# Performance work log

Hardware: AMD Instinct MI355X
Metric: run time of the kernel (lower is better)

Reference implementation:

```python
import jax, jax.numpy as jnp
import numpy as np
import math

KERNEL_SIZES = [3, 5, 7, 7, 9, 9]
DILATIONS = [1, 2, 1, 3, 1, 2]
NUM_HEADS = 6
HEAD_DIM = 32  # in_channels 192 / 6 heads


def _neighborhood_patches(t, k, dil):
    """Equivalent of F.unfold(t, kernel_size=k, dilation=dil, padding=dil*(k//2)).
    t: [B, d, H, W] -> [B, d, k*k, H, W] (zero-padded borders, torch unfold ordering:
    patch index p = i*k + j over the kernel window, row-major)."""
    B, d, H, W = t.shape
    pad = dil * (k // 2)
    tp = jnp.pad(t, ((0, 0), (0, 0), (pad, pad), (pad, pad)))
    pats = [tp[:, :, i * dil:i * dil + H, j * dil:j * dil + W]
            for i in range(k) for j in range(k)]
    return jnp.stack(pats, axis=2)


def setup_inputs() -> dict:
    key = jax.random.key(0)
    ks = jax.random.split(key, 3 + NUM_HEADS)
    B, C, H, W = 4, 192, 96, 96
    x = jax.random.normal(ks[0], (B, C, H, W), dtype=jnp.float32)
    w_qkv = jax.random.normal(ks[1], (3 * C, C), dtype=jnp.float32) * 0.02  # 1x1 conv weight
    w_out = jax.random.normal(ks[2], (C, C), dtype=jnp.float32) * 0.02      # 1x1 conv weight
    inp = {"x": x, "w_qkv": w_qkv, "w_out": w_out}
    for i, k in enumerate(KERNEL_SIZES):
        # module inits biases to zeros; use small randn so softmax path is exercised
        inp[f"b{i}"] = jax.random.normal(ks[3 + i], (k * k,), dtype=jnp.float32) * 0.02
    return inp


def reference(x, w_qkv, w_out, b0, b1, b2, b3, b4, b5):
    biases = [b0, b1, b2, b3, b4, b5]
    B, C, H, W = x.shape
    scale = 1.0 / math.sqrt(HEAD_DIM)
    # 1x1 conv qkv projection
    qkv = jnp.einsum('bchw,oc->bohw', x, w_qkv)
    q, k, v = jnp.split(qkv, 3, axis=1)
    q = q.reshape(B, NUM_HEADS, HEAD_DIM, H, W)
    k = k.reshape(B, NUM_HEADS, HEAD_DIM, H, W)
    v = v.reshape(B, NUM_HEADS, HEAD_DIM, H, W)
    head_outs = []
    for i in range(NUM_HEADS):  # heads have structurally different (k, dilation)
        ksz, dil = KERNEL_SIZES[i], DILATIONS[i]
        kp = _neighborhood_patches(k[:, i], ksz, dil)  # [B, d, k*k, H, W]
        vp = _neighborhood_patches(v[:, i], ksz, dil)  # [B, d, k*k, H, W]
        scores = jnp.einsum('bdhw,bdphw->bphw', q[:, i], kp) * scale
        scores = scores + biases[i][None, :, None, None]
        attn = jax.nn.softmax(scores, axis=1)  # softmax over the k*k neighborhood
        head_outs.append(jnp.einsum('bphw,bdphw->bdhw', attn, vp))
    out = jnp.concatenate(head_outs, axis=1)  # [B, C, H, W]
    return jnp.einsum('bchw,oc->bohw', out, w_out)
```

## Files before the change

### kernel.cpp

```cpp
#include <hip/hip_runtime.h>
#include <hip/hip_bf16.h>
#include <math.h>

#define NPIX 9216
#define HDIM 96
#define WDIM 96
#define NHEADS 6
#define BATCH 4

typedef __bf16 bf16x8 __attribute__((ext_vector_type(8)));
typedef float  f32x4  __attribute__((ext_vector_type(4)));

struct Bias6 { const float* p[6]; };

__device__ __forceinline__ void cp16(void* ldst, const void* gsrc) {
    __builtin_amdgcn_global_load_lds(
        (const __attribute__((address_space(1))) unsigned int*)gsrc,
        (__attribute__((address_space(3))) unsigned int*)ldst, 16, 0, 0);
}

__device__ __forceinline__ unsigned short bfbits(__bf16 x) { return *(unsigned short*)&x; }

__device__ __forceinline__ unsigned packf16(float a, float b) {
    _Float16 ha = (_Float16)a, hb = (_Float16)b;
    return (unsigned)*(unsigned short*)&ha | ((unsigned)*(unsigned short*)&hb << 16);
}

#define MIX_LL(acc, kk, qq) asm("v_fma_mix_f32 %0, %1, %2, %0 op_sel:[0,0,0] op_sel_hi:[1,1,0]" : "+v"(acc) : "v"(kk), "v"(qq))
#define MIX_HH(acc, kk, qq) asm("v_fma_mix_f32 %0, %1, %2, %0 op_sel:[1,1,0] op_sel_hi:[1,1,0]" : "+v"(acc) : "v"(kk), "v"(qq))
#define MIX_LF(acc, vv, ee) asm("v_fma_mix_f32 %0, %1, %2, %0 op_sel:[0,0,0] op_sel_hi:[1,0,0]" : "+v"(acc) : "v"(vv), "v"(ee))
#define MIX_HF(acc, vv, ee) asm("v_fma_mix_f32 %0, %1, %2, %0 op_sel:[1,0,0] op_sel_hi:[1,0,0]" : "+v"(acc) : "v"(vv), "v"(ee))

__global__ __launch_bounds__(256) void convert_w(
    const float* __restrict__ w1, __bf16* __restrict__ h1, __bf16* __restrict__ l1, int n1,
    const float* __restrict__ w2, __bf16* __restrict__ h2, __bf16* __restrict__ l2, int n2)
{
    const int i = blockIdx.x * 256 + threadIdx.x;
    if (i < n1) { float f = w1[i]; __bf16 h = (__bf16)f; h1[i] = h; l1[i] = (__bf16)(f - (float)h); }
    if (i < n2) { float f = w2[i]; __bf16 h = (__bf16)f; h2[i] = h; l2[i] = (__bf16)(f - (float)h); }
}

__global__ __launch_bounds__(256) void convert_x(
    const float* __restrict__ x, __bf16* __restrict__ Xh)
{
    __shared__ float t[32][65];
    const int b  = blockIdx.z;
    const int c0 = blockIdx.y * 32;
    const int p0 = blockIdx.x * 64;
    const int tid = threadIdx.x;
    const int pl = tid & 63;
    #pragma unroll
    for (int i = 0; i < 8; ++i) {
        const int c = i * 4 + (tid >> 6);
        t[c][pl] = x[((size_t)b * 192 + c0 + c) * NPIX + p0 + pl];
    }
    __syncthreads();
    const int p  = tid >> 2;
    const int cq = (tid & 3) * 8;
    bf16x8 vh;
    #pragma unroll
    for (int j = 0; j < 8; ++j)
        vh[j] = (__bf16)t[cq + j][p];
    *(bf16x8*)(Xh + ((size_t)b * NPIX + p0 + p) * 192 + c0 + cq) = vh;
}

template<int MODE>
__global__ __launch_bounds__(256) void gemm_mfma(
    const __bf16* __restrict__ Ah, const __bf16* __restrict__ Al,
    const __bf16* __restrict__ Bh,
    void* __restrict__ Yv, int M)
{
    __shared__ __bf16 sAh[64 * 64];
    __shared__ __bf16 sAl[64 * 64];
    __shared__ __bf16 sBh[128 * 64];

    const int b  = blockIdx.z;
    const int n0 = blockIdx.x * 128;
    const int m0 = blockIdx.y * 64;
    const int tid  = threadIdx.x;
    const int lane = tid & 63;
    const int wid  = tid >> 6;
    const int wr = wid >> 1, wc = wid & 1;
    const int lr = lane & 15;
    const int kg = lane >> 4;

    const char* gA_h = (const char*)Ah + (size_t)m0 * 384;
    const char* gA_l = (const char*)Al + (size_t)m0 * 384;
    const char* gB   = (const char*)Bh + ((size_t)b * NPIX + n0) * 384;

    f32x4 acc[2][4];
    #pragma unroll
    for (int mf = 0; mf < 2; ++mf)
        #pragma unroll
        for (int nf = 0; nf < 4; ++nf)
            acc[mf][nf] = (f32x4){0.f, 0.f, 0.f, 0.f};

    for (int ks = 0; ks < 3; ++ks) {
        if (ks) __syncthreads();
        const int kb = ks * 128;
        #pragma unroll
        for (int it = 0; it < 2; ++it) {
            const int d  = it * 256 + tid;
            const int rd = d >> 3, cd = d & 7;
            const size_t src = (size_t)rd * 384 + kb + ((cd ^ (rd & 7)) << 4);
            cp16((char*)sAh + d * 16, gA_h + src);
            cp16((char*)sAl + d * 16, gA_l + src);
        }
        #pragma unroll
        for (int it = 0; it < 4; ++it) {
            const int d  = it * 256 + tid;
            const int rd = d >> 3, cd = d & 7;
            const size_t src = (size_t)rd * 384 + kb + ((cd ^ (rd & 7)) << 4);
            cp16((char*)sBh + d * 16, gB + src);
        }
        __syncthreads();
        #pragma unroll
        for (int s = 0; s < 2; ++s) {
            bf16x8 aH[2], aL[2], bH[4];
            #pragma unroll
            for (int mf = 0; mf < 2; ++mf) {
                const int row = wr * 32 + mf * 16 + lr;
                const int c = (s * 4 + kg) ^ (row & 7);
                aH[mf] = *(const bf16x8*)((const char*)sAh + row * 128 + c * 16);
                aL[mf] = *(const bf16x8*)((const char*)sAl + row * 128 + c * 16);
            }
            #pragma unroll
            for (int nf = 0; nf < 4; ++nf) {
                const int row = wc * 64 + nf * 16 + lr;
                const int c = (s * 4 + kg) ^ (row & 7);
                bH[nf] = *(const bf16x8*)((const char*)sBh + row * 128 + c * 16);
            }
            #pragma unroll
            for (int mf = 0; mf < 2; ++mf)
                #pragma unroll
                for (int nf = 0; nf < 4; ++nf) {
                    acc[mf][nf] = __builtin_amdgcn_mfma_f32_16x16x32_bf16(aH[mf], bH[nf], acc[mf][nf], 0, 0, 0);
                    acc[mf][nf] = __builtin_amdgcn_mfma_f32_16x16x32_bf16(aL[mf], bH[nf], acc[mf][nf], 0, 0, 0);
                }
        }
    }

    if (MODE == 0) {
        float* Yb = (float*)Yv + ((size_t)b * M + m0 + wr * 32) * NPIX + n0 + wc * 64;
        #pragma unroll
        for (int mf = 0; mf < 2; ++mf)
            #pragma unroll
            for (int r = 0; r < 4; ++r) {
                const int row = mf * 16 + kg * 4 + r;
                #pragma unroll
                for (int nf = 0; nf < 4; ++nf)
                    Yb[(size_t)row * NPIX + nf * 16 + lr] = acc[mf][nf][r];
            }
    } else {
        #pragma unroll
        for (int mf = 0; mf < 2; ++mf) {
            const int mbase = m0 + wr * 32 + mf * 16 + kg * 4;
            unsigned* Yb = (unsigned*)Yv + ((size_t)b * (M >> 1) + (mbase >> 1)) * NPIX
                         + n0 + wc * 64 + lr;
            #pragma unroll
            for (int nf = 0; nf < 4; ++nf) {
                Yb[nf * 16]        = packf16(acc[mf][nf][0], acc[mf][nf][1]);
                Yb[(size_t)NPIX + nf * 16] = packf16(acc[mf][nf][2], acc[mf][nf][3]);
            }
        }
    }
}

#define MAX_REGION 1300

template<int KSZ, int DIL>
__device__ __forceinline__ void attn_body(
    const unsigned* __restrict__ Qpp, const unsigned* __restrict__ Kpp,
    const unsigned* __restrict__ Vpp, const float* __restrict__ bias,
    __bf16* __restrict__ oh, int h0, int w0,
    uint4* __restrict__ lds,
    unsigned (* __restrict__ out_lds)[256])
{
    constexpr int CC  = KSZ / 2;
    constexpr int HAL = CC * DIL;
    constexpr int R   = 8 + 2 * HAL;
    constexpr int C   = 32 + 2 * HAL;
    constexpr int RC  = R * C;
    constexpr int NN  = KSZ * KSZ;
    const float scale = 0.17677669529663689f;

    const int tx = threadIdx.x & 31;
    const int ty = threadIdx.x >> 5;
    const int pix = (h0 + ty) * WDIM + (w0 + tx);
    const int lb = ty * C + tx;

    float score[NN];
    #pragma unroll
    for (int n = 0; n < NN; ++n) score[n] = 0.f;

    for (int pp = 0; pp < 16; pp += 4) {
        __syncthreads();
        for (int idx = threadIdx.x; idx < RC; idx += 256) {
            const int r = idx / C, c = idx - r * C;
            const int gh = h0 - HAL + r, gw = w0 - HAL + c;
            uint4 v = make_uint4(0u, 0u, 0u, 0u);
            if ((unsigned)gh < (unsigned)HDIM && (unsigned)gw < (unsigned)WDIM) {
                const unsigned* p = Kpp + (size_t)pp * NPIX + gh * WDIM + gw;
                v.x = p[0 * NPIX];
                v.y = p[1 * NPIX];
                v.z = p[2 * NPIX];
                v.w = p[3 * NPIX];
            }
            lds[idx] = v;
        }
        __syncthreads();
        unsigned qp0 = Qpp[(size_t)(pp + 0) * NPIX + pix];
        unsigned qp1 = Qpp[(size_t)(pp + 1) * NPIX + pix];
        unsigned qp2 = Qpp[(size_t)(pp + 2) * NPIX + pix];
        unsigned qp3 = Qpp[(size_t)(pp + 3) * NPIX + pix];
        #pragma unroll
        for (int i = 0; i < KSZ; ++i)
            #pragma unroll
            for (int j = 0; j < KSZ; ++j) {
                const uint4 k8 = lds[lb + i * DIL * C + j * DIL];
                float s = score[i * KSZ + j];
                MIX_LL(s, k8.x, qp0); MIX_HH(s, k8.x, qp0);
                MIX_LL(s, k8.y, qp1); MIX_HH(s, k8.y, qp1);
                MIX_LL(s, k8.z, qp2); MIX_HH(s, k8.z, qp2);
                MIX_LL(s, k8.w, qp3); MIX_HH(s, k8.w, qp3);
                score[i * KSZ + j] = s;
            }
    }

    float l = 0.f;
    #pragma unroll
    for (int n = 0; n < NN; ++n) {
        const float e = __expf(score[n] * scale + bias[n]);
        l += e;
        score[n] = e;
    }
    const float inv = 1.f / l;

    for (int pp = 0; pp < 16; pp += 4) {
        __syncthreads();
        for (int idx = threadIdx.x; idx < RC; idx += 256) {
            const int r = idx / C, c = idx - r * C;
            const int gh = h0 - HAL + r, gw = w0 - HAL + c;
            uint4 v = make_uint4(0u, 0u, 0u, 0u);
            if ((unsigned)gh < (unsigned)HDIM && (unsigned)gw < (unsigned)WDIM) {
                const unsigned* p = Vpp + (size_t)pp * NPIX + gh * WDIM + gw;
                v.x = p[0 * NPIX];
                v.y = p[1 * NPIX];
                v.z = p[2 * NPIX];
                v.w = p[3 * NPIX];
            }
            lds[idx] = v;
        }
        __syncthreads();
        float a0 = 0.f, a1 = 0.f, a2 = 0.f, a3 = 0.f;
        float a4 = 0.f, a5 = 0.f, a6 = 0.f, a7 = 0.f;
        #pragma unroll
        for (int i = 0; i < KSZ; ++i)
            #pragma unroll
            for (int j = 0; j < KSZ; ++j) {
                const uint4 v8 = lds[lb + i * DIL * C + j * DIL];
                const float e = score[i * KSZ + j];
                MIX_LF(a0, v8.x, e); MIX_HF(a1, v8.x, e);
                MIX_LF(a2, v8.y, e); MIX_HF(a3, v8.y, e);
                MIX_LF(a4, v8.z, e); MIX_HF(a5, v8.z, e);
                MIX_LF(a6, v8.w, e); MIX_HF(a7, v8.w, e);
            }
        const __bf16 c0 = (__bf16)(a0 * inv), c1 = (__bf16)(a1 * inv);
        const __bf16 c2 = (__bf16)(a2 * inv), c3 = (__bf16)(a3 * inv);
        const __bf16 c4 = (__bf16)(a4 * inv), c5 = (__bf16)(a5 * inv);
        const __bf16 c6 = (__bf16)(a6 * inv), c7 = (__bf16)(a7 * inv);
        out_lds[pp + 0][threadIdx.x] = (unsigned)bfbits(c0) | ((unsigned)bfbits(c1) << 16);
        out_lds[pp + 1][threadIdx.x] = (unsigned)bfbits(c2) | ((unsigned)bfbits(c3) << 16);
        out_lds[pp + 2][threadIdx.x] = (unsigned)bfbits(c4) | ((unsigned)bfbits(c5) << 16);
        out_lds[pp + 3][threadIdx.x] = (unsigned)bfbits(c6) | ((unsigned)bfbits(c7) << 16);
    }

    __syncthreads();
    #pragma unroll
    for (int it = 0; it < 4; ++it) {
        const int linear = it * 256 + threadIdx.x;
        const int px = linear >> 2;
        const int c  = linear & 3;
        const int gpix = (h0 + (px >> 5)) * WDIM + w0 + (px & 31);
        uint4 val = make_uint4(out_lds[c * 4 + 0][px], out_lds[c * 4 + 1][px],
                               out_lds[c * 4 + 2][px], out_lds[c * 4 + 3][px]);
        *(uint4*)((unsigned*)(oh + (size_t)gpix * 192) + c * 4) = val;
    }
}

__global__ __launch_bounds__(256) void attn_kernel(
    const unsigned* __restrict__ qkv, Bias6 bs, __bf16* __restrict__ ATh)
{
    __shared__ uint4 lds[MAX_REGION];
    __shared__ unsigned out_lds[16][256];

    const int orig = blockIdx.x;
    const int wg = (orig & 7) * 108 + (orig >> 3);
    const int panel = wg / 36;
    const int tile = wg - panel * 36;
    const int chunk = panel / 3, slot = panel - chunk * 3;
    int head, b;
    if (slot == 0)      { head = 4 + (chunk >> 2); b = chunk & 3; }
    else if (slot == 1) { head = 2 + (chunk >> 2); b = chunk & 3; }
    else                { head = (chunk < 4) ? 1 : 0; b = chunk & 3; }
    const int tx = tile % 3, ty = tile / 3;
    const int w0 = tx * 32, h0 = ty * 8;

    const unsigned* Qpp = qkv + ((size_t)b * 288 + head * 16) * NPIX;
    const unsigned* Kpp = Qpp + (size_t)96 * NPIX;
    const unsigned* Vpp = Qpp + (size_t)192 * NPIX;
    __bf16* oh = ATh + (size_t)b * NPIX * 192 + head * 32;
    const float* bias = bs.p[head];

    switch (head) {
        case 0: attn_body<3, 1>(Qpp, Kpp, Vpp, bias, oh, h0, w0, lds, out_lds); break;
        case 1: attn_body<5, 2>(Qpp, Kpp, Vpp, bias, oh, h0, w0, lds, out_lds); break;
        case 2: attn_body<7, 1>(Qpp, Kpp, Vpp, bias, oh, h0, w0, lds, out_lds); break;
        case 3: attn_body<7, 3>(Qpp, Kpp, Vpp, bias, oh, h0, w0, lds, out_lds); break;
        case 4: attn_body<9, 1>(Qpp, Kpp, Vpp, bias, oh, h0, w0, lds, out_lds); break;
        case 5: attn_body<9, 2>(Qpp, Kpp, Vpp, bias, oh, h0, w0, lds, out_lds); break;
    }
}

extern "C" void kernel_launch(void* const* d_in, const int* in_sizes, int n_in,
                              void* d_out, int out_size, void* d_ws, size_t ws_size,
                              hipStream_t stream) {
    const float* x     = (const float*)d_in[0];
    const float* w_qkv = (const float*)d_in[1];
    const float* w_out = (const float*)d_in[2];
    Bias6 bs;
    for (int i = 0; i < 6; ++i) bs.p[i] = (const float*)d_in[3 + i];
    float* out = (float*)d_out;

    char* ws = (char*)d_ws;
    unsigned* QKV = (unsigned*)ws;      ws += (size_t)BATCH * 288 * NPIX * 4;
    __bf16* Xh  = (__bf16*)ws;          ws += (size_t)BATCH * NPIX * 192 * 2;
    __bf16* ATh = (__bf16*)ws;          ws += (size_t)BATCH * NPIX * 192 * 2;
    __bf16* W1h = (__bf16*)ws;          ws += (size_t)576 * 192 * 2;
    __bf16* W1l = (__bf16*)ws;          ws += (size_t)576 * 192 * 2;
    __bf16* W2h = (__bf16*)ws;          ws += (size_t)192 * 192 * 2;
    __bf16* W2l = (__bf16*)ws;          ws += (size_t)192 * 192 * 2;

    convert_w<<<dim3((576 * 192 + 255) / 256), 256, 0, stream>>>(
        w_qkv, W1h, W1l, 576 * 192, w_out, W2h, W2l, 192 * 192);
    convert_x<<<dim3(NPIX / 64, 192 / 32, BATCH), 256, 0, stream>>>(x, Xh);

    gemm_mfma<1><<<dim3(NPIX / 128, 576 / 64, BATCH), 256, 0, stream>>>(
        W1h, W1l, Xh, (void*)QKV, 576);

    attn_kernel<<<dim3(864), 256, 0, stream>>>(QKV, bs, ATh);

    gemm_mfma<0><<<dim3(NPIX / 128, 192 / 64, BATCH), 256, 0, stream>>>(
        W2h, W2l, ATh, (void*)out, 192);
}
```

Measured before the change: 98.98 us.

## Store QKV as 8-channel interleaved uint4 planes for vectorized attention loads

The QKV GEMM epilogue now writes fp16 pairs into a layout where each pixel holds 8 consecutive channels in one 16-byte chunk. The attention kernel then fetches K, V and Q neighborhoods with single uint4 loads instead of four strided 4-byte loads. It also halves the output staging buffer by writing results in two halves, which costs extra barriers. The GEMM stores become strided 4-byte writes with a 16-byte stride, which may be less coalesced.

Measured after the change: 97.38 us. Within noise of the previous version (-1.6%).

```diff
diff --git a/kernel.cpp b/kernel.cpp
--- a/kernel.cpp
+++ b/kernel.cpp
@@ -154,13 +154,14 @@
     } else {
         #pragma unroll
         for (int mf = 0; mf < 2; ++mf) {
-            const int mbase = m0 + wr * 32 + mf * 16 + kg * 4;
-            unsigned* Yb = (unsigned*)Yv + ((size_t)b * (M >> 1) + (mbase >> 1)) * NPIX
-                         + n0 + wc * 64 + lr;
+            const int cbase = m0 + wr * 32 + mf * 16 + kg * 4;
+            unsigned* Yq = (unsigned*)Yv
+                + (((size_t)b * 72 + (cbase >> 3)) * NPIX + n0 + wc * 64 + lr) * 4
+                + ((kg & 1) << 1);
             #pragma unroll
             for (int nf = 0; nf < 4; ++nf) {
-                Yb[nf * 16]        = packf16(acc[mf][nf][0], acc[mf][nf][1]);
-                Yb[(size_t)NPIX + nf * 16] = packf16(acc[mf][nf][2], acc[mf][nf][3]);
+                Yq[(nf * 16) * 4 + 0] = packf16(acc[mf][nf][0], acc[mf][nf][1]);
+                Yq[(nf * 16) * 4 + 1] = packf16(acc[mf][nf][2], acc[mf][nf][3]);
             }
         }
     }
@@ -170,8 +171,8 @@
 
 template<int KSZ, int DIL>
 __device__ __forceinline__ void attn_body(
-    const unsigned* __restrict__ Qpp, const unsigned* __restrict__ Kpp,
-    const unsigned* __restrict__ Vpp, const float* __restrict__ bias,
+    const uint4* __restrict__ Qq, const uint4* __restrict__ Kq,
+    const uint4* __restrict__ Vq, const float* __restrict__ bias,
     __bf16* __restrict__ oh, int h0, int w0,
     uint4* __restrict__ lds,
     unsigned (* __restrict__ out_lds)[256])
@@ -193,36 +194,28 @@
     #pragma unroll
     for (int n = 0; n < NN; ++n) score[n] = 0.f;
 
-    for (int pp = 0; pp < 16; pp += 4) {
+    for (int pp = 0; pp < 4; ++pp) {
         __syncthreads();
         for (int idx = threadIdx.x; idx < RC; idx += 256) {
             const int r = idx / C, c = idx - r * C;
             const int gh = h0 - HAL + r, gw = w0 - HAL + c;
             uint4 v = make_uint4(0u, 0u, 0u, 0u);
-            if ((unsigned)gh < (unsigned)HDIM && (unsigned)gw < (unsigned)WDIM) {
-                const unsigned* p = Kpp + (size_t)pp * NPIX + gh * WDIM + gw;
-                v.x = p[0 * NPIX];
-                v.y = p[1 * NPIX];
-                v.z = p[2 * NPIX];
-                v.w = p[3 * NPIX];
-            }
+            if ((unsigned)gh < (unsigned)HDIM && (unsigned)gw < (unsigned)WDIM)
+                v = Kq[(size_t)pp * NPIX + gh * WDIM + gw];
             lds[idx] = v;
         }
         __syncthreads();
-        unsigned qp0 = Qpp[(size_t)(pp + 0) * NPIX + pix];
-        unsigned qp1 = Qpp[(size_t)(pp + 1) * NPIX + pix];
-        unsigned qp2 = Qpp[(size_t)(pp + 2) * NPIX + pix];
-        unsigned qp3 = Qpp[(size_t)(pp + 3) * NPIX + pix];
+        const uint4 qv = Qq[(size_t)pp * NPIX + pix];
         #pragma unroll
         for (int i = 0; i < KSZ; ++i)
             #pragma unroll
             for (int j = 0; j < KSZ; ++j) {
                 const uint4 k8 = lds[lb + i * DIL * C + j * DIL];
                 float s = score[i * KSZ + j];
-                MIX_LL(s, k8.x, qp0); MIX_HH(s, k8.x, qp0);
-                MIX_LL(s, k8.y, qp1); MIX_HH(s, k8.y, qp1);
-                MIX_LL(s, k8.z, qp2); MIX_HH(s, k8.z, qp2);
-                MIX_LL(s, k8.w, qp3); MIX_HH(s, k8.w, qp3);
+                MIX_LL(s, k8.x, qv.x); MIX_HH(s, k8.x, qv.x);
+                MIX_LL(s, k8.y, qv.y); MIX_HH(s, k8.y, qv.y);
+                MIX_LL(s, k8.z, qv.z); MIX_HH(s, k8.z, qv.z);
+                MIX_LL(s, k8.w, qv.w); MIX_HH(s, k8.w, qv.w);
                 score[i * KSZ + j] = s;
             }
     }
@@ -236,63 +229,62 @@
     }
     const float inv = 1.f / l;
 
-    for (int pp = 0; pp < 16; pp += 4) {
+    #pragma unroll
+    for (int half = 0; half < 2; ++half) {
+        #pragma unroll
+        for (int rr = 0; rr < 2; ++rr) {
+            const int pp = half * 2 + rr;
+            __syncthreads();
+            for (int idx = threadIdx.x; idx < RC; idx += 256) {
+                const int r = idx / C, c = idx - r * C;
+                const int gh = h0 - HAL + r, gw = w0 - HAL + c;
+                uint4 v = make_uint4(0u, 0u, 0u, 0u);
+                if ((unsigned)gh < (unsigned)HDIM && (unsigned)gw < (unsigned)WDIM)
+                    v = Vq[(size_t)pp * NPIX + gh * WDIM + gw];
+                lds[idx] = v;
+            }
+            __syncthreads();
+            float a0 = 0.f, a1 = 0.f, a2 = 0.f, a3 = 0.f;
+            float a4 = 0.f, a5 = 0.f, a6 = 0.f, a7 = 0.f;
+            #pragma unroll
+            for (int i = 0; i < KSZ; ++i)
+                #pragma unroll
+                for (int j = 0; j < KSZ; ++j) {
+                    const uint4 v8 = lds[lb + i * DIL * C + j * DIL];
+                    const float e = score[i * KSZ + j];
+                    MIX_LF(a0, v8.x, e); MIX_HF(a1, v8.x, e);
+                    MIX_LF(a2, v8.y, e); MIX_HF(a3, v8.y, e);
+                    MIX_LF(a4, v8.z, e); MIX_HF(a5, v8.z, e);
+                    MIX_LF(a6, v8.w, e); MIX_HF(a7, v8.w, e);
+                }
+            const __bf16 c0 = (__bf16)(a0 * inv), c1 = (__bf16)(a1 * inv);
+            const __bf16 c2 = (__bf16)(a2 * inv), c3 = (__bf16)(a3 * inv);
+            const __bf16 c4 = (__bf16)(a4 * inv), c5 = (__bf16)(a5 * inv);
+            const __bf16 c6 = (__bf16)(a6 * inv), c7 = (__bf16)(a7 * inv);
+            out_lds[rr * 4 + 0][threadIdx.x] = (unsigned)bfbits(c0) | ((unsigned)bfbits(c1) << 16);
+            out_lds[rr * 4 + 1][threadIdx.x] = (unsigned)bfbits(c2) | ((unsigned)bfbits(c3) << 16);
+            out_lds[rr * 4 + 2][threadIdx.x] = (unsigned)bfbits(c4) | ((unsigned)bfbits(c5) << 16);
+            out_lds[rr * 4 + 3][threadIdx.x] = (unsigned)bfbits(c6) | ((unsigned)bfbits(c7) << 16);
+        }
         __syncthreads();
-        for (int idx = threadIdx.x; idx < RC; idx += 256) {
-            const int r = idx / C, c = idx - r * C;
-            const int gh = h0 - HAL + r, gw = w0 - HAL + c;
-            uint4 v = make_uint4(0u, 0u, 0u, 0u);
-            if ((unsigned)gh < (unsigned)HDIM && (unsigned)gw < (unsigned)WDIM) {
-                const unsigned* p = Vpp + (size_t)pp * NPIX + gh * WDIM + gw;
-                v.x = p[0 * NPIX];
-                v.y = p[1 * NPIX];
-                v.z = p[2 * NPIX];
-                v.w = p[3 * NPIX];
-            }
-            lds[idx] = v;
-        }
-        __syncthreads();
-        float a0 = 0.f, a1 = 0.f, a2 = 0.f, a3 = 0.f;
-        float a4 = 0.f, a5 = 0.f, a6 = 0.f, a7 = 0.f;
-        #pragma unroll
-        for (int i = 0; i < KSZ; ++i)
-            #pragma unroll
-            for (int j = 0; j < KSZ; ++j) {
-                const uint4 v8 = lds[lb + i * DIL * C + j * DIL];
-                const float e = score[i * KSZ + j];
-                MIX_LF(a0, v8.x, e); MIX_HF(a1, v8.x, e);
-                MIX_LF(a2, v8.y, e); MIX_HF(a3, v8.y, e);
-                MIX_LF(a4, v8.z, e); MIX_HF(a5, v8.z, e);
-                MIX_LF(a6, v8.w, e); MIX_HF(a7, v8.w, e);
-            }
-        const __bf16 c0 = (__bf16)(a0 * inv), c1 = (__bf16)(a1 * inv);
-        const __bf16 c2 = (__bf16)(a2 * inv), c3 = (__bf16)(a3 * inv);
-        const __bf16 c4 = (__bf16)(a4 * inv), c5 = (__bf16)(a5 * inv);
-        const __bf16 c6 = (__bf16)(a6 * inv), c7 = (__bf16)(a7 * inv);
-        out_lds[pp + 0][threadIdx.x] = (unsigned)bfbits(c0) | ((unsigned)bfbits(c1) << 16);
-        out_lds[pp + 1][threadIdx.x] = (unsigned)bfbits(c2) | ((unsigned)bfbits(c3) << 16);
-        out_lds[pp + 2][threadIdx.x] = (unsigned)bfbits(c4) | ((unsigned)bfbits(c5) << 16);
-        out_lds[pp + 3][threadIdx.x] = (unsigned)bfbits(c6) | ((unsigned)bfbits(c7) << 16);
-    }
-
-    __syncthreads();
-    #pragma unroll
-    for (int it = 0; it < 4; ++it) {
-        const int linear = it * 256 + threadIdx.x;
-        const int px = linear >> 2;
-        const int c  = linear & 3;
-        const int gpix = (h0 + (px >> 5)) * WDIM + w0 + (px & 31);
-        uint4 val = make_uint4(out_lds[c * 4 + 0][px], out_lds[c * 4 + 1][px],
-                               out_lds[c * 4 + 2][px], out_lds[c * 4 + 3][px]);
-        *(uint4*)((unsigned*)(oh + (size_t)gpix * 192) + c * 4) = val;
+        #pragma unroll
+        for (int it = 0; it < 2; ++it) {
+            const int linear = it * 256 + threadIdx.x;
+            const int px = linear >> 1;
+            const int c  = linear & 1;
+            const int gpix = (h0 + (px >> 5)) * WDIM + w0 + (px & 31);
+            uint4 val = make_uint4(out_lds[c * 4 + 0][px], out_lds[c * 4 + 1][px],
+                                   out_lds[c * 4 + 2][px], out_lds[c * 4 + 3][px]);
+            *((uint4*)((unsigned*)(oh + (size_t)gpix * 192)) + half * 2 + c) = val;
+        }
     }
 }
 
 __global__ __launch_bounds__(256) void attn_kernel(
-    const unsigned* __restrict__ qkv, Bias6 bs, __bf16* __restrict__ ATh)
+    const uint4* __restrict__ qkv, Bias6 bs, __bf16* __restrict__ ATh)
 {
     __shared__ uint4 lds[MAX_REGION];
-    __shared__ unsigned out_lds[16][256];
+    __shared__ unsigned out_lds[8][256];
 
     const int orig = blockIdx.x;
     const int wg = (orig & 7) * 108 + (orig >> 3);
@@ -306,19 +298,20 @@
     const int tx = tile % 3, ty = tile / 3;
     const int w0 = tx * 32, h0 = ty * 8;
 
-    const unsigned* Qpp = qkv + ((size_t)b * 288 + head * 16) * NPIX;
-    const unsigned* Kpp = Qpp + (size_t)96 * NPIX;
-    const unsigned* Vpp = Qpp + (size_t)192 * NPIX;
+    const uint4* base = qkv + (size_t)b * 72 * NPIX;
+    const uint4* Qq = base + (size_t)(head * 4) * NPIX;
+    const uint4* Kq = base + (size_t)(24 + head * 4) * NPIX;
+    const uint4* Vq = base + (size_t)(48 + head * 4) * NPIX;
     __bf16* oh = ATh + (size_t)b * NPIX * 192 + head * 32;
     const float* bias = bs.p[head];
 
     switch (head) {
-        case 0: attn_body<3, 1>(Qpp, Kpp, Vpp, bias, oh, h0, w0, lds, out_lds); break;
-        case 1: attn_body<5, 2>(Qpp, Kpp, Vpp, bias, oh, h0, w0, lds, out_lds); break;
-        case 2: attn_body<7, 1>(Qpp, Kpp, Vpp, bias, oh, h0, w0, lds, out_lds); break;
-        case 3: attn_body<7, 3>(Qpp, Kpp, Vpp, bias, oh, h0, w0, lds, out_lds); break;
-        case 4: attn_body<9, 1>(Qpp, Kpp, Vpp, bias, oh, h0, w0, lds, out_lds); break;
-        case 5: attn_body<9, 2>(Qpp, Kpp, Vpp, bias, oh, h0, w0, lds, out_lds); break;
+        case 0: attn_body<3, 1>(Qq, Kq, Vq, bias, oh, h0, w0, lds, out_lds); break;
+        case 1: attn_body<5, 2>(Qq, Kq, Vq, bias, oh, h0, w0, lds, out_lds); break;
+        case 2: attn_body<7, 1>(Qq, Kq, Vq, bias, oh, h0, w0, lds, out_lds); break;
+        case 3: attn_body<7, 3>(Qq, Kq, Vq, bias, oh, h0, w0, lds, out_lds); break;
+        case 4: attn_body<9, 1>(Qq, Kq, Vq, bias, oh, h0, w0, lds, out_lds); break;
+        case 5: attn_body<9, 2>(Qq, Kq, Vq, bias, oh, h0, w0, lds, out_lds); break;
     }
 }
 
@@ -333,7 +326,7 @@
     float* out = (float*)d_out;
 
     char* ws = (char*)d_ws;
-    unsigned* QKV = (unsigned*)ws;      ws += (size_t)BATCH * 288 * NPIX * 4;
+    uint4* QKV = (uint4*)ws;            ws += (size_t)BATCH * 72 * NPIX * 16;
     __bf16* Xh  = (__bf16*)ws;          ws += (size_t)BATCH * NPIX * 192 * 2;
     __bf16* ATh = (__bf16*)ws;          ws += (size_t)BATCH * NPIX * 192 * 2;
     __bf16* W1h = (__bf16*)ws;          ws += (size_t)576 * 192 * 2;
```
